# Performance work log

Measured on AMD Instinct MI355X. Metric: run time of the kernel, lower is better.

The kernel has to match this reference:

```python
import jax, jax.numpy as jnp
import numpy as np
from jax import lax

B, S, D, H, TMAX = 8, 512, 256, 4, 20
DH = D // H
LAMBDA = 1e-3
V_TH = 1.0


def setup_inputs() -> dict:
    key = jax.random.key(0)
    ks = jax.random.split(key, 10)
    sc = lambda n: 1.0 / np.sqrt(n)
    f32 = jnp.float32
    return {
        "x": jax.random.normal(ks[0], (B, S, D), f32),
        "Wq": (jax.random.normal(ks[1], (D, D), f32) * sc(D)),
        "Wk": (jax.random.normal(ks[2], (D, D), f32) * sc(D)),
        "Wv": (jax.random.normal(ks[3], (D, D), f32) * sc(D)),
        "Wo": (jax.random.normal(ks[4], (D, D), f32) * sc(D)),
        "bo": jnp.zeros((D,), f32),
        "Wg1": (jax.random.normal(ks[5], (D, 32), f32) * sc(D)),
        "bg1": jnp.zeros((32,), f32),
        "Wg2": (jax.random.normal(ks[6], (32, 1), f32) * sc(32)),
        "bg2": jnp.zeros((1,), f32),
        "alpha_q": jnp.asarray(np.exp(-1 / 5.0), f32),
        "beta_q": jnp.asarray(np.exp(-1 / 20.0), f32),
        "alpha_k": jnp.asarray(np.exp(-1 / 5.0), f32),
        "beta_k": jnp.asarray(np.exp(-1 / 20.0), f32),
        "alpha_v": jnp.asarray(np.exp(-1 / 5.0), f32),
        "beta_v": jnp.asarray(np.exp(-1 / 20.0), f32),
    }


def _lif_spikes(x, alpha, beta, Ti):
    """LIF recurrence with CONSTANT input x per step, sequential only over T.
    x: [B,S,D], Ti: [B,S] int. Returns spikes [B,S,TMAX,D], zeroed for t >= Ti
    (equivalent to the original per-(b,s) loop that only runs Ti steps,
    since the recurrence is causal)."""
    zeros = jnp.zeros_like(x)
    tmask = jnp.arange(TMAX)

    def step(carry, t):
        v, i = carry
        i = alpha * i + x
        v = beta * v + i
        spk = (v >= V_TH).astype(x.dtype)
        v = v * (1.0 - spk)  # v_reset = 0
        spk_out = spk * (t < Ti).astype(x.dtype)[..., None]
        return (v, i), spk_out

    _, spks = lax.scan(step, (zeros, zeros), tmask)
    return jnp.moveaxis(spks, 0, 2)  # [B,S,T,D]


def reference(x, Wq, Wk, Wv, Wo, bo, Wg1, bg1, Wg2, bg2,
              alpha_q, beta_q, alpha_k, beta_k, alpha_v, beta_v):
    q = x @ Wq
    k = x @ Wk
    v = x @ Wv
    # adaptive window gate -> Ti in [1, TMAX]
    gate = jax.nn.sigmoid(jax.nn.relu(x @ Wg1 + bg1) @ Wg2 + bg2)[..., 0]  # [B,S]
    Ti = jnp.clip(jnp.ceil(gate * TMAX), 1, TMAX).astype(jnp.int32)
    q_spk = _lif_spikes(q, alpha_q, beta_q, Ti)  # [B,S,T,D]
    k_spk = _lif_spikes(k, alpha_k, beta_k, Ti)
    v_spk = _lif_spikes(v, alpha_v, beta_v, Ti)
    qh = q_spk.reshape(B, S, TMAX, H, DH)
    kh = k_spk.reshape(B, S, TMAX, H, DH)
    vh = v_spk.reshape(B, S, TMAX, H, DH)
    scale = DH ** -0.5
    Sraw = jnp.einsum('bithd,bjthd->bhij', qh, kh) * scale  # [B,H,S,S]
    W = jax.nn.softmax(Sraw, axis=-1)
    v_mean = vh.mean(axis=2)  # [B,S,H,DH] (mean over full T, zeros beyond Ti)
    out = jnp.einsum('bhij,bjhd->bihd', W, v_mean).reshape(B, S, D)
    out = out @ Wo + bo
    reg = LAMBDA * Ti.astype(jnp.float32).mean()
    return out, reg, Ti, W
```

## Files before the change

### kernel.cpp

```cpp
#include <hip/hip_runtime.h>
#include <hip/hip_bf16.h>

typedef unsigned long long u64;
typedef unsigned short u16;
typedef __attribute__((ext_vector_type(8))) short short8;
typedef __attribute__((ext_vector_type(4))) float float4_t;

#define BB 8
#define SS 512
#define DD 256
#define HH 4
#define TT 20
#define BS (BB*SS)

#define REG_OFF (BS*DD)
#define TI_OFF  (REG_OFF+1)
#define W_OFF   (TI_OFF+BS)

static __device__ __forceinline__ u16 f2bf(float f) {
    __hip_bfloat16 h = __float2bfloat16(f);
    return *reinterpret_cast<u16*>(&h);
}

__global__ __launch_bounds__(256) void k_gate(
    const float* __restrict__ x,
    const float* __restrict__ Wg1, const float* __restrict__ bg1,
    const float* __restrict__ Wg2, const float* __restrict__ bg2,
    float* __restrict__ ti_out)
{
    const int tid  = threadIdx.x;
    const int tok  = blockIdx.x * 4 + (tid >> 6);
    const int lane = tid & 63;
    const int c    = lane & 31;
    const int half = lane >> 5;

    const float* xr = x + (size_t)tok*DD + half*128;
    const float* wg = Wg1 + (size_t)half*128*32 + c;
    float acc = 0.f;
    #pragma unroll 4
    for (int i = 0; i < 32; ++i) {
        float4_t xv = *reinterpret_cast<const float4_t*>(xr + i*4);
        acc += xv.x * wg[(i*4+0)*32] + xv.y * wg[(i*4+1)*32]
             + xv.z * wg[(i*4+2)*32] + xv.w * wg[(i*4+3)*32];
    }
    acc += __shfl_xor(acc, 32, 64);
    acc += bg1[c];
    float hrelu = acc > 0.f ? acc : 0.f;
    float term  = hrelu * Wg2[c];
    #pragma unroll
    for (int msk = 16; msk >= 1; msk >>= 1) term += __shfl_xor(term, msk, 64);
    if (lane == 0) {
        float g  = term + bg2[0];
        float sg = 1.f / (1.f + expf(-g));
        int ti = (int)ceilf(sg * (float)TT);
        ti = ti < 1 ? 1 : (ti > TT ? TT : ti);
        ti_out[tok] = (float)ti;
    }
}

__global__ __launch_bounds__(256) void k_proj_lif(
    const float* __restrict__ x, const float* __restrict__ Wq,
    const float* __restrict__ Wk, const float* __restrict__ Wv,
    const float* __restrict__ aq, const float* __restrict__ bq_,
    const float* __restrict__ ak, const float* __restrict__ bk_,
    const float* __restrict__ av, const float* __restrict__ bv_,
    const float* __restrict__ ti_in,
    u64* __restrict__ qpack, u64* __restrict__ kpack,
    u16* __restrict__ vmb)
{
    __shared__ __align__(16) union {
        float xt[DD][8];
        float red[4][8][DD];
    } sm;
    __shared__ int til[8];
    const int tid  = threadIdx.x;
    const int proj = blockIdx.y;
    const int tok0 = blockIdx.x * 8;
    const int w = tid >> 6, l = tid & 63;

    #pragma unroll
    for (int m = 0; m < 8; ++m) sm.xt[tid][m] = x[(size_t)(tok0+m)*DD + tid];
    if (tid < 8) til[tid] = (int)ti_in[tok0 + tid];
    __syncthreads();

    const float* W    = proj == 0 ? Wq  : (proj == 1 ? Wk  : Wv);
    const float alpha = proj == 0 ? *aq : (proj == 1 ? *ak : *av);
    const float beta  = proj == 0 ? *bq_: (proj == 1 ? *bk_: *bv_);

    float4_t a[8];
    #pragma unroll
    for (int i = 0; i < 8; ++i) a[i] = (float4_t){0.f, 0.f, 0.f, 0.f};

    const float* Wp = W + (size_t)(w*64)*DD + l*4;
    #pragma unroll 4
    for (int r0 = 0; r0 < 64; ++r0) {
        float4_t wf = *reinterpret_cast<const float4_t*>(Wp + (size_t)r0*DD);
        int r = (w << 6) + r0;
        float4_t x0 = *reinterpret_cast<const float4_t*>(&sm.xt[r][0]);
        float4_t x1 = *reinterpret_cast<const float4_t*>(&sm.xt[r][4]);
        a[0] += wf*x0.x; a[1] += wf*x0.y; a[2] += wf*x0.z; a[3] += wf*x0.w;
        a[4] += wf*x1.x; a[5] += wf*x1.y; a[6] += wf*x1.z; a[7] += wf*x1.w;
    }
    __syncthreads();
    #pragma unroll
    for (int i = 0; i < 8; ++i)
        *reinterpret_cast<float4_t*>(&sm.red[w][i][l*4]) = a[i];
    __syncthreads();

    float val[8];
    #pragma unroll
    for (int i = 0; i < 8; ++i)
        val[i] = (sm.red[0][i][tid] + sm.red[1][i][tid])
               + (sm.red[2][i][tid] + sm.red[3][i][tid]);

    const int h = w;
    if (proj < 2) {
        u64* pack = (proj == 0) ? qpack : kpack;
        for (int i = 0; i < 8; ++i) {
            const int ti = til[i];
            float vv = 0.f, cur = 0.f;
            u64 myw = 0ull;
            #pragma unroll
            for (int t = 0; t < TT; ++t) {
                cur = alpha*cur + val[i];
                vv  = beta*vv + cur;
                bool s = (vv >= 1.f);
                u64 bal = __ballot(s);
                if (s) vv = 0.f;
                if (l == t && t < ti) myw = bal;
            }
            if (l < TT)
                pack[((size_t)(tok0+i)*HH + h)*TT + l] = myw;
        }
    } else {
        for (int i = 0; i < 8; ++i) {
            const int ti = til[i];
            float vv = 0.f, cur = 0.f, cnt = 0.f;
            #pragma unroll
            for (int t = 0; t < TT; ++t) {
                cur = alpha*cur + val[i];
                vv  = beta*vv + cur;
                bool s = (vv >= 1.f);
                if (s) { vv = 0.f; if (t < ti) cnt += 1.f; }
            }
            vmb[(size_t)(tok0+i)*DD + tid] = f2bf(cnt * 0.05f);
        }
    }
}

__global__ __launch_bounds__(256) void k_attn(
    const u64* __restrict__ qpack, const u64* __restrict__ kpack,
    const u16* __restrict__ vmb,
    float* __restrict__ Wout, float* __restrict__ attn)
{
    __shared__ u64 ql[16][TT];
    __shared__ __align__(16) u16 CP[16*SS];
    const int tid  = threadIdx.x;
    const int tile = blockIdx.x & 31;
    const int h    = (blockIdx.x >> 5) & 3;
    const int b    = blockIdx.x >> 7;
    const int i0   = tile * 16;
    const int lane = tid & 63, wv = tid >> 6;

    for (int idx = tid; idx < 16*TT; idx += 256) {
        int i = idx / TT, t = idx - i*TT;
        ql[i][t] = qpack[((size_t)(b*SS + i0 + i)*HH + h)*TT + t];
    }

    u64 kr0[TT], kr1[TT];
    {
        const u64* kp0 = &kpack[((size_t)(b*SS + tid      )*HH + h)*TT];
        const u64* kp1 = &kpack[((size_t)(b*SS + tid + 256)*HH + h)*TT];
        #pragma unroll
        for (int t = 0; t < TT; ++t) { kr0[t] = kp0[t]; kr1[t] = kp1[t]; }
    }
    __syncthreads();

    for (int i = 0; i < 16; ++i) {
        int c0 = 0, c1 = 0;
        #pragma unroll
        for (int t = 0; t < TT; ++t) {
            u64 q = ql[i][t];
            c0 += __popcll(q & kr0[t]);
            c1 += __popcll(q & kr1[t]);
        }
        CP[i*SS + tid]       = (u16)c0;
        CP[i*SS + tid + 256] = (u16)c1;
    }
    __syncthreads();

    for (int rr = 0; rr < 4; ++rr) {
        const int i = wv*4 + rr;
        float sv[8];
        float m = -1e30f;
        #pragma unroll
        for (int k2 = 0; k2 < 8; ++k2) {
            sv[k2] = (float)CP[i*SS + lane + 64*k2] * 0.125f;
            m = fmaxf(m, sv[k2]);
        }
        #pragma unroll
        for (int msk = 32; msk >= 1; msk >>= 1) m = fmaxf(m, __shfl_xor(m, msk, 64));
        float sum = 0.f;
        #pragma unroll
        for (int k2 = 0; k2 < 8; ++k2) { sv[k2] = expf(sv[k2] - m); sum += sv[k2]; }
        #pragma unroll
        for (int msk = 32; msk >= 1; msk >>= 1) sum += __shfl_xor(sum, msk, 64);
        float inv = 1.f / sum;
        size_t wbase = ((size_t)((b*HH + h)*SS) + i0 + i) * SS;
        #pragma unroll
        for (int k2 = 0; k2 < 8; ++k2) {
            int j = lane + 64*k2;
            float wval = sv[k2] * inv;
            Wout[wbase + j] = wval;
            CP[(i*SS + j) ^ ((i & 7) << 3)] = f2bf(wval);
        }
    }
    __syncthreads();

    const int n0 = wv * 16;
    const int mr = lane & 15;
    const int g  = lane >> 4;
    float4_t acc = {0.f, 0.f, 0.f, 0.f};
    const u16* vb_base = vmb + (size_t)b*SS*DD + h*64 + n0 + mr;
    for (int ks = 0; ks < 16; ++ks) {
        int k = ks*32 + g*8;
        int aidx = (mr*SS + k) ^ ((mr & 7) << 3);
        short8 a = *reinterpret_cast<const short8*>(&CP[aidx]);
        union { u16 u[8]; short8 v; } bu;
        const u16* vb = vb_base + (size_t)k*DD;
        #pragma unroll
        for (int j = 0; j < 8; ++j) bu.u[j] = vb[(size_t)j*DD];
        acc = __builtin_amdgcn_mfma_f32_16x16x32_bf16(a, bu.v, acc, 0, 0, 0);
    }
    #pragma unroll
    for (int r = 0; r < 4; ++r) {
        int row = g*4 + r;
        attn[(size_t)(b*SS + i0 + row)*DD + h*64 + n0 + mr] = acc[r];
    }
}

__global__ __launch_bounds__(256) void k_outproj(
    const float* __restrict__ attn, const float* __restrict__ Wo,
    const float* __restrict__ bo, const float* __restrict__ ti,
    float* __restrict__ out)
{
    __shared__ __align__(16) union {
        float xt[DD][8];
        float red[4][8][DD];
    } sm;
    __shared__ float ps[4];
    const int tid  = threadIdx.x;
    const int tok0 = blockIdx.x * 8;
    const int w = tid >> 6, l = tid & 63;

    #pragma unroll
    for (int m = 0; m < 8; ++m) sm.xt[tid][m] = attn[(size_t)(tok0+m)*DD + tid];
    __syncthreads();

    float4_t a[8];
    #pragma unroll
    for (int i = 0; i < 8; ++i) a[i] = (float4_t){0.f, 0.f, 0.f, 0.f};
    const float* Wp = Wo + (size_t)(w*64)*DD + l*4;
    #pragma unroll 4
    for (int r0 = 0; r0 < 64; ++r0) {
        float4_t wf = *reinterpret_cast<const float4_t*>(Wp + (size_t)r0*DD);
        int r = (w << 6) + r0;
        float4_t x0 = *reinterpret_cast<const float4_t*>(&sm.xt[r][0]);
        float4_t x1 = *reinterpret_cast<const float4_t*>(&sm.xt[r][4]);
        a[0] += wf*x0.x; a[1] += wf*x0.y; a[2] += wf*x0.z; a[3] += wf*x0.w;
        a[4] += wf*x1.x; a[5] += wf*x1.y; a[6] += wf*x1.z; a[7] += wf*x1.w;
    }
    __syncthreads();
    #pragma unroll
    for (int i = 0; i < 8; ++i)
        *reinterpret_cast<float4_t*>(&sm.red[w][i][l*4]) = a[i];
    __syncthreads();

    float bb = bo[tid];
    #pragma unroll
    for (int i = 0; i < 8; ++i) {
        float v = (sm.red[0][i][tid] + sm.red[1][i][tid])
                + (sm.red[2][i][tid] + sm.red[3][i][tid]);
        out[(size_t)(tok0+i)*DD + tid] = v + bb;
    }

    if (blockIdx.x == 0) {
        float s = 0.f;
        for (int m = 0; m < 16; ++m) s += ti[m*256 + tid];
        #pragma unroll
        for (int msk = 32; msk >= 1; msk >>= 1) s += __shfl_xor(s, msk, 64);
        if ((tid & 63) == 0) ps[tid >> 6] = s;
        __syncthreads();
        if (tid == 0) out[REG_OFF] = 1e-3f * (ps[0]+ps[1]+ps[2]+ps[3]) / 4096.f;
    }
}

extern "C" void kernel_launch(void* const* d_in, const int* in_sizes, int n_in,
                              void* d_out, int out_size, void* d_ws, size_t ws_size,
                              hipStream_t stream)
{
    (void)in_sizes; (void)n_in; (void)out_size; (void)ws_size;
    const float* x   = (const float*)d_in[0];
    const float* Wq  = (const float*)d_in[1];
    const float* Wk  = (const float*)d_in[2];
    const float* Wv  = (const float*)d_in[3];
    const float* Wo  = (const float*)d_in[4];
    const float* bo  = (const float*)d_in[5];
    const float* Wg1 = (const float*)d_in[6];
    const float* bg1 = (const float*)d_in[7];
    const float* Wg2 = (const float*)d_in[8];
    const float* bg2 = (const float*)d_in[9];
    const float* aq  = (const float*)d_in[10];
    const float* bq  = (const float*)d_in[11];
    const float* ak  = (const float*)d_in[12];
    const float* bk  = (const float*)d_in[13];
    const float* av  = (const float*)d_in[14];
    const float* bv  = (const float*)d_in[15];
    float* out = (float*)d_out;

    u64* qp = (u64*)d_ws;
    u64* kp = qp + (size_t)BS*HH*TT;
    u16* vmb = (u16*)(kp + (size_t)BS*HH*TT);
    float* attnbuf = (float*)(vmb + (size_t)BS*DD);

    k_gate<<<1024, 256, 0, stream>>>(x, Wg1, bg1, Wg2, bg2, out + TI_OFF);
    dim3 gproj(512, 3);
    k_proj_lif<<<gproj, 256, 0, stream>>>(x, Wq, Wk, Wv,
        aq, bq, ak, bk, av, bv, out + TI_OFF, qp, kp, vmb);
    k_attn<<<1024, 256, 0, stream>>>(qp, kp, vmb, out + W_OFF, attnbuf);
    k_outproj<<<512, 256, 0, stream>>>(attnbuf, Wo, bo, out + TI_OFF, out);
}
```

Measured before the change: 102.9 us.

## Transpose v-mean layout and move output projection to bf16 MFMA

Stores the spike-count v-mean buffer transposed so the attention kernel loads its B fragment with one 16-byte vector load instead of eight strided scalar loads. The attention output is written as bf16, and a new prep kernel transposes Wo into bf16, so the output projection can run on MFMA matrix instructions in place of the scalar FP32 FMA loop with its LDS reduction. This adds an extra small kernel launch and lowers the precision of the out-projection inputs to bf16.

```diff
diff --git a/kernel.cpp b/kernel.cpp
--- a/kernel.cpp
+++ b/kernel.cpp
@@ -58,6 +58,18 @@
     }
 }
 
+__global__ __launch_bounds__(256) void k_prep_wo(
+    const float* __restrict__ Wo, u16* __restrict__ WoT)
+{
+    const int e  = blockIdx.x * 256 + threadIdx.x;
+    const int n  = e & 255;
+    const int k0 = (e >> 8) * 8;
+    u16 a[8];
+    #pragma unroll
+    for (int j = 0; j < 8; ++j) a[j] = f2bf(Wo[(size_t)(k0+j)*DD + n]);
+    *reinterpret_cast<short8*>(&WoT[(size_t)n*DD + k0]) = *reinterpret_cast<short8*>(a);
+}
+
 __global__ __launch_bounds__(256) void k_proj_lif(
     const float* __restrict__ x, const float* __restrict__ Wq,
     const float* __restrict__ Wk, const float* __restrict__ Wv,
@@ -66,7 +78,7 @@
     const float* __restrict__ av, const float* __restrict__ bv_,
     const float* __restrict__ ti_in,
     u64* __restrict__ qpack, u64* __restrict__ kpack,
-    u16* __restrict__ vmb)
+    u16* __restrict__ vmbT)
 {
     __shared__ __align__(16) union {
         float xt[DD][8];
@@ -133,6 +145,7 @@
                 pack[((size_t)(tok0+i)*HH + h)*TT + l] = myw;
         }
     } else {
+        u16 tmp[8];
         for (int i = 0; i < 8; ++i) {
             const int ti = til[i];
             float vv = 0.f, cur = 0.f, cnt = 0.f;
@@ -143,15 +156,17 @@
                 bool s = (vv >= 1.f);
                 if (s) { vv = 0.f; if (t < ti) cnt += 1.f; }
             }
-            vmb[(size_t)(tok0+i)*DD + tid] = f2bf(cnt * 0.05f);
-        }
+            tmp[i] = f2bf(cnt * 0.05f);
+        }
+        *reinterpret_cast<short8*>(&vmbT[(size_t)tid*BS + tok0]) =
+            *reinterpret_cast<short8*>(tmp);
     }
 }
 
 __global__ __launch_bounds__(256) void k_attn(
     const u64* __restrict__ qpack, const u64* __restrict__ kpack,
-    const u16* __restrict__ vmb,
-    float* __restrict__ Wout, float* __restrict__ attn)
+    const u16* __restrict__ vmbT,
+    float* __restrict__ Wout, u16* __restrict__ attnb)
 {
     __shared__ u64 ql[16][TT];
     __shared__ __align__(16) u16 CP[16*SS];
@@ -221,67 +236,57 @@
     const int mr = lane & 15;
     const int g  = lane >> 4;
     float4_t acc = {0.f, 0.f, 0.f, 0.f};
-    const u16* vb_base = vmb + (size_t)b*SS*DD + h*64 + n0 + mr;
+    const u16* vbT = vmbT + (size_t)(h*64 + n0 + mr)*BS + b*SS;
     for (int ks = 0; ks < 16; ++ks) {
         int k = ks*32 + g*8;
         int aidx = (mr*SS + k) ^ ((mr & 7) << 3);
-        short8 a = *reinterpret_cast<const short8*>(&CP[aidx]);
-        union { u16 u[8]; short8 v; } bu;
-        const u16* vb = vb_base + (size_t)k*DD;
-        #pragma unroll
-        for (int j = 0; j < 8; ++j) bu.u[j] = vb[(size_t)j*DD];
-        acc = __builtin_amdgcn_mfma_f32_16x16x32_bf16(a, bu.v, acc, 0, 0, 0);
+        short8 afrag = *reinterpret_cast<const short8*>(&CP[aidx]);
+        short8 bfrag = *reinterpret_cast<const short8*>(vbT + k);
+        acc = __builtin_amdgcn_mfma_f32_16x16x32_bf16(afrag, bfrag, acc, 0, 0, 0);
     }
     #pragma unroll
     for (int r = 0; r < 4; ++r) {
         int row = g*4 + r;
-        attn[(size_t)(b*SS + i0 + row)*DD + h*64 + n0 + mr] = acc[r];
+        attnb[(size_t)(b*SS + i0 + row)*DD + h*64 + n0 + mr] = f2bf(acc[r]);
     }
 }
 
 __global__ __launch_bounds__(256) void k_outproj(
-    const float* __restrict__ attn, const float* __restrict__ Wo,
+    const u16* __restrict__ attnb, const u16* __restrict__ WoT,
     const float* __restrict__ bo, const float* __restrict__ ti,
     float* __restrict__ out)
 {
-    __shared__ __align__(16) union {
-        float xt[DD][8];
-        float red[4][8][DD];
-    } sm;
     __shared__ float ps[4];
     const int tid  = threadIdx.x;
-    const int tok0 = blockIdx.x * 8;
-    const int w = tid >> 6, l = tid & 63;
-
-    #pragma unroll
-    for (int m = 0; m < 8; ++m) sm.xt[tid][m] = attn[(size_t)(tok0+m)*DD + tid];
-    __syncthreads();
-
-    float4_t a[8];
-    #pragma unroll
-    for (int i = 0; i < 8; ++i) a[i] = (float4_t){0.f, 0.f, 0.f, 0.f};
-    const float* Wp = Wo + (size_t)(w*64)*DD + l*4;
+    const int tok0 = blockIdx.x * 16;
+    const int lane = tid & 63;
+    const int wv   = tid >> 6;
+    const int mr   = lane & 15;
+    const int g    = lane >> 4;
+
+    float4_t acc[4];
+    #pragma unroll
+    for (int f = 0; f < 4; ++f) acc[f] = (float4_t){0.f, 0.f, 0.f, 0.f};
+
+    const size_t arow = (size_t)(tok0 + mr)*DD + g*8;
     #pragma unroll 4
-    for (int r0 = 0; r0 < 64; ++r0) {
-        float4_t wf = *reinterpret_cast<const float4_t*>(Wp + (size_t)r0*DD);
-        int r = (w << 6) + r0;
-        float4_t x0 = *reinterpret_cast<const float4_t*>(&sm.xt[r][0]);
-        float4_t x1 = *reinterpret_cast<const float4_t*>(&sm.xt[r][4]);
-        a[0] += wf*x0.x; a[1] += wf*x0.y; a[2] += wf*x0.z; a[3] += wf*x0.w;
-        a[4] += wf*x1.x; a[5] += wf*x1.y; a[6] += wf*x1.z; a[7] += wf*x1.w;
-    }
-    __syncthreads();
-    #pragma unroll
-    for (int i = 0; i < 8; ++i)
-        *reinterpret_cast<float4_t*>(&sm.red[w][i][l*4]) = a[i];
-    __syncthreads();
-
-    float bb = bo[tid];
-    #pragma unroll
-    for (int i = 0; i < 8; ++i) {
-        float v = (sm.red[0][i][tid] + sm.red[1][i][tid])
-                + (sm.red[2][i][tid] + sm.red[3][i][tid]);
-        out[(size_t)(tok0+i)*DD + tid] = v + bb;
+    for (int ks = 0; ks < 8; ++ks) {
+        const int k = ks*32;
+        short8 a = *reinterpret_cast<const short8*>(&attnb[arow + k]);
+        #pragma unroll
+        for (int f = 0; f < 4; ++f) {
+            const size_t brow = (size_t)(wv*64 + f*16 + mr)*DD + k + g*8;
+            short8 b = *reinterpret_cast<const short8*>(&WoT[brow]);
+            acc[f] = __builtin_amdgcn_mfma_f32_16x16x32_bf16(a, b, acc[f], 0, 0, 0);
+        }
+    }
+    #pragma unroll
+    for (int f = 0; f < 4; ++f) {
+        const int col = wv*64 + f*16 + mr;
+        const float bb = bo[col];
+        #pragma unroll
+        for (int r = 0; r < 4; ++r)
+            out[(size_t)(tok0 + g*4 + r)*DD + col] = acc[f][r] + bb;
     }
 
     if (blockIdx.x == 0) {
@@ -318,15 +323,17 @@
     const float* bv  = (const float*)d_in[15];
     float* out = (float*)d_out;
 
-    u64* qp = (u64*)d_ws;
-    u64* kp = qp + (size_t)BS*HH*TT;
-    u16* vmb = (u16*)(kp + (size_t)BS*HH*TT);
-    float* attnbuf = (float*)(vmb + (size_t)BS*DD);
+    u64* qp    = (u64*)d_ws;
+    u64* kp    = qp + (size_t)BS*HH*TT;
+    u16* vmbT  = (u16*)(kp + (size_t)BS*HH*TT);
+    u16* attnb = vmbT + (size_t)BS*DD;
+    u16* WoT   = attnb + (size_t)BS*DD;
 
     k_gate<<<1024, 256, 0, stream>>>(x, Wg1, bg1, Wg2, bg2, out + TI_OFF);
+    k_prep_wo<<<32, 256, 0, stream>>>(Wo, WoT);
     dim3 gproj(512, 3);
     k_proj_lif<<<gproj, 256, 0, stream>>>(x, Wq, Wk, Wv,
-        aq, bq, ak, bk, av, bv, out + TI_OFF, qp, kp, vmb);
-    k_attn<<<1024, 256, 0, stream>>>(qp, kp, vmb, out + W_OFF, attnbuf);
-    k_outproj<<<512, 256, 0, stream>>>(attnbuf, Wo, bo, out + TI_OFF, out);
-}
+        aq, bq, ak, bk, av, bv, out + TI_OFF, qp, kp, vmbT);
+    k_attn<<<1024, 256, 0, stream>>>(qp, kp, vmbT, out + W_OFF, attnb);
+    k_outproj<<<256, 256, 0, stream>>>(attnb, WoT, bo, out + TI_OFF, out);
+}
```

New measurement: 104.0 us. About the same (+1.1%).
